# Performance work log

Measured on AMD Instinct MI355X. Metric: run time of the kernel, lower is better.

## Reference

```python
import jax, jax.numpy as jnp
import numpy as np

N = 6000
E = 192000
H = 128
NUM_HEADS = 4

def _segsum(x, idx, n):
    return jax.ops.segment_sum(x, idx, num_segments=n)

def _gcn_encode(x, edges, W0, b0, Ws, bs):
    n = x.shape[0]
    sl = jnp.arange(n, dtype=edges.dtype)
    row = jnp.concatenate([edges[0], sl])  # source
    col = jnp.concatenate([edges[1], sl])  # target (aggregation)
    deg = _segsum(jnp.ones_like(col, dtype=x.dtype), col, n)
    dinv = jax.lax.rsqrt(deg)  # deg >= 1 thanks to self loops
    norm = (dinv[row] * dinv[col])[:, None]
    def layer(h, W, b):
        hw = h @ W
        agg = _segsum(hw[row] * norm, col, n)
        return jax.nn.relu(agg + b)
    h = layer(x, W0, b0)
    for i in range(Ws.shape[0]):
        h = layer(h, Ws[i], bs[i])
    return h

def setup_inputs() -> dict:
    key = jax.random.key(0)
    ks = jax.random.split(key, 24)
    def lin(k, fan_in, shape):
        return jax.random.normal(k, shape, dtype=jnp.float32) / np.sqrt(fan_in)
    return {
        'x_resting': jax.random.normal(ks[0], (N, 3), dtype=jnp.float32),
        'x_rigid': jax.random.normal(ks[1], (N, 3), dtype=jnp.float32),
        'edge_resting': jax.random.randint(ks[2], (2, E), 0, N, dtype=jnp.int32),
        'edge_rigid': jax.random.randint(ks[3], (2, E), 0, N, dtype=jnp.int32),
        'Wr0': lin(ks[4], 3, (3, H)), 'br0': jnp.zeros((H,), jnp.float32),
        'Wr': lin(ks[5], H, (2, H, H)), 'br': jnp.zeros((2, H), jnp.float32),
        'Wg0': lin(ks[6], 3, (3, H)), 'bg0': jnp.zeros((H,), jnp.float32),
        'Wg': lin(ks[7], H, (2, H, H)), 'bg': jnp.zeros((2, H), jnp.float32),
        'Wa': lin(ks[8], H, (NUM_HEADS, H, H)), 'ba': jnp.zeros((NUM_HEADS, H), jnp.float32),
        'Wd0': lin(ks[9], H * (NUM_HEADS + 1), (H * (NUM_HEADS + 1), H)), 'bd0': jnp.zeros((H,), jnp.float32),
        'Wd': lin(ks[10], H, (2, H, H)), 'bd': jnp.zeros((2, H), jnp.float32),
        'Wout': lin(ks[11], H, (H, 3)), 'bout': jnp.zeros((3,), jnp.float32),
    }

def reference(x_resting, x_rigid, edge_resting, edge_rigid,
              Wr0, br0, Wr, br, Wg0, bg0, Wg, bg,
              Wa, ba, Wd0, bd0, Wd, bd, Wout, bout):
    xr = _gcn_encode(x_resting, edge_resting, Wr0, br0, Wr, br)  # (N,H)
    xg = _gcn_encode(x_rigid, edge_rigid, Wg0, bg0, Wg, bg)      # (N,H)

    def head(W, b):
        q = xr @ W + b            # (N,H)
        k = xg @ W + b            # (N,H)
        attn = jax.nn.softmax(q @ k.T, axis=-1)  # (N,N) dense per head
        return attn @ xg          # (N,H)
    heads = jax.vmap(head)(Wa, ba)                       # (heads,N,H)
    pooled = heads.transpose(1, 0, 2).reshape(xr.shape[0], -1)  # (N, heads*H)

    h = jnp.concatenate([xr, pooled], axis=-1)  # (N, H*(heads+1))
    h = jax.nn.relu(h @ Wd0 + bd0)
    for i in range(Wd.shape[0]):
        h = jax.nn.relu(h @ Wd[i] + bd[i])
    return h @ Wout + bout  # (N, 3) deformed positions
```

## Files before the change

### kernel.cpp

```cpp
#include <hip/hip_runtime.h>
#include <math.h>

#define N_NODES 6000
#define N_EDGES 192000
#define H 128
#define NHEADS 4
#define HCAT 640
#define NPAD 6016
#define NTILES 188
#define QBLK 24

typedef unsigned short ushort_t;
typedef __attribute__((ext_vector_type(8))) short short8;
typedef __attribute__((ext_vector_type(16))) float f32x16;

__device__ __forceinline__ void bf16split(float x, ushort_t& hi, ushort_t& lo) {
    unsigned ub = __float_as_uint(x);
    unsigned hb = ub & 0xffff0000u;
    float l = x - __uint_as_float(hb);
    hi = (ushort_t)(hb >> 16);
    lo = (ushort_t)(__float_as_uint(l) >> 16);
}

__device__ __forceinline__ void gll16(const ushort_t* g, ushort_t* l) {
    __builtin_amdgcn_global_load_lds((const __attribute__((address_space(1))) void*)g,
                                     (__attribute__((address_space(3))) void*)l, 16, 0, 0);
}

__global__ void zero_ints(int* p, int n) {
    int i = blockIdx.x * 256 + threadIdx.x;
    if (i < n) p[i] = 0;
}

__global__ void hist2(const int* __restrict__ eA, const int* __restrict__ eB,
                      int* __restrict__ cnt) {
    int e = blockIdx.x * 256 + threadIdx.x;
    int z = blockIdx.y;
    const int* edges = z ? eB : eA;
    if (e < N_EDGES) atomicAdd(&cnt[z * N_NODES + edges[N_EDGES + e]], 1);
}

__global__ __launch_bounds__(1024)
void scan2(const int* __restrict__ cnt_all, int* __restrict__ rs_all) {
    __shared__ int ps[1024];
    int z = blockIdx.x;
    const int* cnt = cnt_all + z * N_NODES;
    int* row_start = rs_all + z * (N_NODES + 1);
    int t = threadIdx.x;
    int base = t * 6;
    int local[6];
    int s = 0;
#pragma unroll
    for (int j = 0; j < 6; ++j) {
        int idx = base + j;
        int v = (idx < N_NODES) ? cnt[idx] : 0;
        local[j] = s;
        s += v;
    }
    ps[t] = s;
    __syncthreads();
    for (int off = 1; off < 1024; off <<= 1) {
        int v = (t >= off) ? ps[t - off] : 0;
        __syncthreads();
        ps[t] += v;
        __syncthreads();
    }
    int ex = (t > 0) ? ps[t - 1] : 0;
#pragma unroll
    for (int j = 0; j < 6; ++j) {
        int idx = base + j;
        if (idx < N_NODES) row_start[idx] = ex + local[j];
    }
    if (t == 1023) row_start[N_NODES] = ps[1023];
}

__global__ void dinv_kernel(const int* __restrict__ cnt, float* __restrict__ dinv, int n) {
    int i = blockIdx.x * 256 + threadIdx.x;
    if (i < n) dinv[i] = rsqrtf((float)(cnt[i] + 1));
}

__global__ void place2(const int* __restrict__ eA, const int* __restrict__ eB,
                       const int* __restrict__ rs_all, int* __restrict__ cur_all,
                       int* __restrict__ eslot_all) {
    int e = blockIdx.x * 256 + threadIdx.x;
    int z = blockIdx.y;
    const int* edges = z ? eB : eA;
    if (e < N_EDGES) {
        int tg = edges[N_EDGES + e];
        int p = atomicAdd(&cur_all[z * N_NODES + tg], 1);
        eslot_all[(size_t)z * N_EDGES + rs_all[z * (N_NODES + 1) + tg] + p] = e;
    }
}

__global__ __launch_bounds__(256)
void gather_x3(const float* __restrict__ xA, const float* __restrict__ xB,
               const int* __restrict__ eA, const int* __restrict__ eB,
               const int* __restrict__ eslot_all, const int* __restrict__ rs_all,
               const float* __restrict__ dinv_all,
               float* __restrict__ outA, float* __restrict__ outB) {
    int z = blockIdx.y;
    int n = blockIdx.x * 256 + threadIdx.x;
    if (n >= N_NODES) return;
    const int* edges = z ? eB : eA;
    const int* eslot = eslot_all + (size_t)z * N_EDGES;
    const int* row_start = rs_all + z * (N_NODES + 1);
    const float* x = z ? xB : xA;
    const float* dv = dinv_all + z * N_NODES;
    float* out = z ? outB : outA;
    float di = dv[n];
    float a0 = x[n * 3 + 0] * di * di;
    float a1 = x[n * 3 + 1] * di * di;
    float a2 = x[n * 3 + 2] * di * di;
    int s0 = row_start[n], s1 = row_start[n + 1];
    for (int i = s0; i < s1; ++i) {
        int e = eslot[i];
        int s = edges[e];
        float nr = dv[s] * di;
        a0 += x[s * 3 + 0] * nr;
        a1 += x[s * 3 + 1] * nr;
        a2 += x[s * 3 + 2] * nr;
    }
    out[n * 3 + 0] = a0; out[n * 3 + 1] = a1; out[n * 3 + 2] = a2;
}

__global__ __launch_bounds__(256)
void gcn_gemm2(const float* __restrict__ hinA, const float* __restrict__ hinB,
               const float* __restrict__ WA, const float* __restrict__ WB,
               float* __restrict__ hwA, float* __restrict__ hwB, int in_dim,
               const float* __restrict__ bA, const float* __restrict__ bB, int do_relu) {
    __shared__ float xs[16 * H];
    int z = blockIdx.y;
    const float* hin = z ? hinB : hinA;
    const float* W = z ? WB : WA;
    float* hw = z ? hwB : hwA;
    const float* b = z ? bB : bA;
    int n0 = blockIdx.x * 16;
    int t = threadIdx.x;
    int f = t & (H - 1);
    int g = t >> 7;
    for (int i = t; i < 16 * H; i += 256) {
        int r = i >> 7, c = i & (H - 1);
        xs[i] = (c < in_dim) ? hin[(size_t)(n0 + r) * in_dim + c] : 0.f;
    }
    __syncthreads();
    float acc[8];
#pragma unroll
    for (int j = 0; j < 8; ++j) acc[j] = 0.f;
    for (int d = 0; d < in_dim; ++d) {
        float w = W[d * H + f];
#pragma unroll
        for (int j = 0; j < 8; ++j) acc[j] += xs[(g * 8 + j) * H + d] * w;
    }
    if (do_relu) {
        float bias = b[f];
#pragma unroll
        for (int j = 0; j < 8; ++j)
            hw[(size_t)(n0 + g * 8 + j) * H + f] = fmaxf(acc[j] + bias, 0.f);
    } else {
#pragma unroll
        for (int j = 0; j < 8; ++j) hw[(size_t)(n0 + g * 8 + j) * H + f] = acc[j];
    }
}

__global__ __launch_bounds__(H)
void gather2(const int* __restrict__ eA, const int* __restrict__ eB,
             const int* __restrict__ eslot_all, const int* __restrict__ rs_all,
             const float* __restrict__ hwA, const float* __restrict__ hwB,
             const float* __restrict__ dinv_all,
             const float* __restrict__ bA, const float* __restrict__ bB,
             float* __restrict__ outA, float* __restrict__ outB, int osA, int osB) {
    __shared__ int ssrc[128];
    __shared__ float snrm[128];
    int z = blockIdx.y;
    const int* edges = z ? eB : eA;
    const int* eslot = eslot_all + (size_t)z * N_EDGES;
    const int* row_start = rs_all + z * (N_NODES + 1);
    const float* hw = z ? hwB : hwA;
    const float* dinv = dinv_all + z * N_NODES;
    const float* b = z ? bB : bA;
    float* out = z ? outB : outA;
    int ostride = z ? osB : osA;

    int tg = blockIdx.x, f = threadIdx.x;
    int s0 = row_start[tg], s1 = row_start[tg + 1];
    float di = dinv[tg];
    float acc = hw[(size_t)tg * H + f] * di * di;
    for (int base = s0; base < s1; base += 128) {
        int cnt = min(128, s1 - base);
        __syncthreads();
        if (f < cnt) {
            int e = eslot[base + f];
            int s = edges[e];
            ssrc[f] = s;
            snrm[f] = dinv[s] * di;
        }
        __syncthreads();
        for (int i = 0; i < cnt; ++i)
            acc += hw[(size_t)ssrc[i] * H + f] * snrm[i];
    }
    float v = acc + b[f];
    out[(size_t)tg * ostride + f] = v > 0.f ? v : 0.f;
}

__global__ __launch_bounds__(256)
void qk_kernel2(const float* __restrict__ qs, int qstride, const float* __restrict__ xg,
                const float* __restrict__ Wa, const float* __restrict__ ba,
                ushort_t* __restrict__ Qh, ushort_t* __restrict__ Ql,
                ushort_t* __restrict__ Khs, ushort_t* __restrict__ Kls) {
    __shared__ float xs[2][16][H];
    int n0 = blockIdx.x * 16, head = blockIdx.y;
    int t = threadIdx.x;
    int f = t & (H - 1);
    int g = t >> 7;
    for (int i = t; i < 2 * 16 * H; i += 256) {
        int which = i >> 11;
        int rem = i & 2047;
        int row = rem >> 7, col = rem & 127;
        xs[which][row][col] = which ? xg[(size_t)(n0 + row) * H + col]
                                    : qs[(size_t)(n0 + row) * qstride + col];
    }
    __syncthreads();
    const float* W = Wa + (size_t)head * H * H;
    float bias = ba[head * H + f];
    float acc[16];
#pragma unroll
    for (int j = 0; j < 16; ++j) acc[j] = bias;
    for (int d = 0; d < H; ++d) {
        float w = W[d * H + f];
#pragma unroll
        for (int j = 0; j < 16; ++j) acc[j] += xs[g][j][d] * w;
    }
#pragma unroll
    for (int j = 0; j < 16; ++j) {
        int n = n0 + j;
        ushort_t hi, lo;
        bf16split(acc[j], hi, lo);
        if (g == 0) {
            size_t idx = ((size_t)(head * N_NODES + n) << 7) + f;
            Qh[idx] = hi; Ql[idx] = lo;
        } else {
            int pos = (((f >> 3) ^ (n & 15)) << 3) + (f & 7);
            size_t idx = ((size_t)(head * NPAD + n) << 7) + pos;
            Khs[idx] = hi; Kls[idx] = lo;
        }
    }
}

__global__ void zero_pad_k(ushort_t* __restrict__ Khs, ushort_t* __restrict__ Kls) {
    int i = blockIdx.x * 256 + threadIdx.x;
    if (i < NHEADS * 16 * H) {
        int head = i / (16 * H);
        int rest = i - head * 16 * H;
        int n = N_NODES + (rest >> 7);
        int f = rest & 127;
        size_t idx = ((size_t)(head * NPAD + n) << 7) + f;
        Khs[idx] = 0; Kls[idx] = 0;
    }
}

__global__ __launch_bounds__(128)
void cvt_vt(const float* __restrict__ xg, ushort_t* __restrict__ Vth, ushort_t* __restrict__ Vtl) {
    __shared__ float vs[32][129];
    int t0 = blockIdx.x;
    int t = threadIdx.x;
    for (int c = t; c < 32 * 32; c += 128) {
        int row = c >> 5, col4 = (c & 31) << 2;
        int n = t0 * 32 + row;
        float4 v = (n < N_NODES) ? *(const float4*)&xg[(size_t)n * H + col4]
                                 : float4{0.f, 0.f, 0.f, 0.f};
        vs[row][col4 + 0] = v.x; vs[row][col4 + 1] = v.y;
        vs[row][col4 + 2] = v.z; vs[row][col4 + 3] = v.w;
    }
    __syncthreads();
    int d = t;
    size_t base = ((size_t)t0 * H + d) * 32;
#pragma unroll
    for (int oc = 0; oc < 4; ++oc) {
        int cc = oc ^ (d & 3);
        unsigned uh[4], ul[4];
#pragma unroll
        for (int j = 0; j < 4; ++j) {
            ushort_t h0, l0, h1, l1;
            bf16split(vs[cc * 8 + 2 * j][d], h0, l0);
            bf16split(vs[cc * 8 + 2 * j + 1][d], h1, l1);
            uh[j] = (unsigned)h0 | ((unsigned)h1 << 16);
            ul[j] = (unsigned)l0 | ((unsigned)l1 << 16);
        }
        *(uint4*)&Vth[base + oc * 8] = make_uint4(uh[0], uh[1], uh[2], uh[3]);
        *(uint4*)&Vtl[base + oc * 8] = make_uint4(ul[0], ul[1], ul[2], ul[3]);
    }
}

__global__ __launch_bounds__(512, 2)
void attn_mfma5(const ushort_t* __restrict__ Qh, const ushort_t* __restrict__ Ql,
                const ushort_t* __restrict__ Khs, const ushort_t* __restrict__ Kls,
                const ushort_t* __restrict__ Vth, const ushort_t* __restrict__ Vtl,
                float* __restrict__ Opart, float* __restrict__ mlpart, int tps) {
    __shared__ ushort_t lds[2][4][4096];
    const int head = blockIdx.y;
    const int sp = blockIdx.z;
    const int t = threadIdx.x;
    const int lane = t & 63;
    const int w = t >> 6;
    const int r = lane & 31;
    const int h = lane >> 5;
    const int q0w = blockIdx.x * 256 + w * 32;

    int t_begin = sp * tps;
    int t_end = t_begin + tps; if (t_end > NTILES) t_end = NTILES;

    const size_t kbase = (size_t)head * NPAD * H;
    const int lo8 = t * 8;

    int qr = q0w + r; if (qr > N_NODES - 1) qr = N_NODES - 1;
    const size_t qbase = ((size_t)(head * N_NODES + qr)) << 7;
    short8 qfh[8], qfl[8];
#pragma unroll
    for (int s = 0; s < 8; ++s) {
        qfh[s] = *(const short8*)&Qh[qbase + 16 * s + 8 * h];
        qfl[s] = *(const short8*)&Ql[qbase + 16 * s + 8 * h];
    }

    f32x16 O[4];
#pragma unroll
    for (int sub = 0; sub < 4; ++sub)
#pragma unroll
        for (int i = 0; i < 16; ++i) O[sub][i] = 0.f;
    float mrun = -1e30f, lrun = 0.f;

    {
        size_t off = (size_t)t_begin * 4096 + lo8;
        gll16(Khs + kbase + off, &lds[0][0][lo8]);
        gll16(Kls + kbase + off, &lds[0][1][lo8]);
        gll16(Vth + off, &lds[0][2][lo8]);
        gll16(Vtl + off, &lds[0][3][lo8]);
    }

    for (int it = t_begin; it < t_end; ++it) {
        const int b = (it - t_begin) & 1;
        __syncthreads();
        {
            int nt = it + 1; if (nt >= t_end) nt = t_begin;
            size_t off = (size_t)nt * 4096 + lo8;
            gll16(Khs + kbase + off, &lds[b ^ 1][0][lo8]);
            gll16(Kls + kbase + off, &lds[b ^ 1][1][lo8]);
            gll16(Vth + off, &lds[b ^ 1][2][lo8]);
            gll16(Vtl + off, &lds[b ^ 1][3][lo8]);
        }
        const ushort_t* lKh = &lds[b][0][0];
        const ushort_t* lKl = &lds[b][1][0];
        const ushort_t* lVh = &lds[b][2][0];
        const ushort_t* lVl = &lds[b][3][0];

        f32x16 acc;
#pragma unroll
        for (int i = 0; i < 16; ++i) acc[i] = 0.f;
        const int krow = r * H;
#pragma unroll
        for (int s = 0; s < 8; ++s) {
            int cc = ((2 * s + h) ^ (r & 15)) << 3;
            short8 ah = *(const short8*)&lKh[krow + cc];
            short8 al = *(const short8*)&lKl[krow + cc];
            acc = __builtin_amdgcn_mfma_f32_32x32x16_bf16(ah, qfh[s], acc, 0, 0, 0);
            acc = __builtin_amdgcn_mfma_f32_32x32x16_bf16(ah, qfl[s], acc, 0, 0, 0);
            acc = __builtin_amdgcn_mfma_f32_32x32x16_bf16(al, qfh[s], acc, 0, 0, 0);
        }

        float sv[16];
#pragma unroll
        for (int i = 0; i < 16; ++i) sv[i] = acc[i];
        int klim = N_NODES - (it << 5);
        if (klim < 32) {
#pragma unroll
            for (int i = 0; i < 16; ++i) {
                int row = (i & 3) + 8 * (i >> 2) + 4 * h;
                if (row >= klim) sv[i] = -1e30f;
            }
        }
        float tmax = sv[0];
#pragma unroll
        for (int i = 1; i < 16; ++i) tmax = fmaxf(tmax, sv[i]);
        tmax = fmaxf(tmax, __shfl_xor(tmax, 32));
        float mnew = fmaxf(mrun, tmax);
        float p[16];
        float psum = 0.f;
#pragma unroll
        for (int i = 0; i < 16; ++i) { p[i] = __expf(sv[i] - mnew); psum += p[i]; }

        if (__ballot(mnew > mrun)) {
            float alpha = __expf(mrun - mnew);
            lrun *= alpha;
#pragma unroll
            for (int i = 0; i < 16; ++i) {
                int rowq = (i & 3) + 8 * (i >> 2) + 4 * h;
                float a = __shfl(alpha, rowq);
#pragma unroll
                for (int sub = 0; sub < 4; ++sub) O[sub][i] *= a;
            }
        }
        lrun += psum;
        mrun = mnew;

        float pr[16];
#pragma unroll
        for (int i = 0; i < 16; ++i) pr[i] = __shfl_xor(p[i], 32);
        short8 aPh[2], aPl[2];
#pragma unroll
        for (int s2 = 0; s2 < 2; ++s2) {
#pragma unroll
            for (int j = 0; j < 8; ++j) {
                int c = j & 3;
                float v;
                if (j < 4) v = (h == 0) ? p[c + 8 * s2] : pr[c + 8 * s2 + 4];
                else       v = (h == 1) ? p[c + 8 * s2 + 4] : pr[c + 8 * s2];
                unsigned ub = __float_as_uint(v);
                unsigned hb = ub & 0xffff0000u;
                float lo = v - __uint_as_float(hb);
                aPh[s2][j] = (short)(hb >> 16);
                aPl[s2][j] = (short)(__float_as_uint(lo) >> 16);
            }
        }

#pragma unroll
        for (int sub = 0; sub < 4; ++sub) {
            const int vrow = (32 * sub + r) * 32;
#pragma unroll
            for (int s2 = 0; s2 < 2; ++s2) {
                int cc = (((2 * s2 + h) ^ (r & 3)) << 3);
                short8 bh = *(const short8*)&lVh[vrow + cc];
                short8 bl = *(const short8*)&lVl[vrow + cc];
                O[sub] = __builtin_amdgcn_mfma_f32_32x32x16_bf16(aPh[s2], bh, O[sub], 0, 0, 0);
                O[sub] = __builtin_amdgcn_mfma_f32_32x32x16_bf16(aPh[s2], bl, O[sub], 0, 0, 0);
                O[sub] = __builtin_amdgcn_mfma_f32_32x32x16_bf16(aPl[s2], bh, O[sub], 0, 0, 0);
            }
        }
    }

    lrun += __shfl_xor(lrun, 32);

    float* Ob = Opart + (size_t)(sp * NHEADS + head) * NPAD * H;
#pragma unroll
    for (int i = 0; i < 16; ++i) {
        int rowq = (i & 3) + 8 * (i >> 2) + 4 * h;
        int qg = q0w + rowq;
        if (qg < N_NODES) {
            float* dst = &Ob[(size_t)qg * H + r];
#pragma unroll
            for (int sub = 0; sub < 4; ++sub) dst[32 * sub] = O[sub][i];
        }
    }
    if (h == 0 && q0w + r < N_NODES) {
        float2* ml = (float2*)mlpart;
        ml[(size_t)(sp * NHEADS + head) * NPAD + q0w + r] = make_float2(mrun, lrun);
    }
}

__global__ __launch_bounds__(256)
void attn_combine(const float* __restrict__ Opart, const float* __restrict__ mlpart,
                  float* __restrict__ hcat, int ns) {
    int idx = blockIdx.x * 256 + threadIdx.x;
    if (idx >= NHEADS * N_NODES * (H / 4)) return;
    int head = idx / (N_NODES * (H / 4));
    int rest = idx - head * N_NODES * (H / 4);
    int q = rest >> 5;
    int d4 = (rest & 31) << 2;
    const float2* ml = (const float2*)mlpart;
    float m = -1e30f;
    for (int s = 0; s < ns; ++s)
        m = fmaxf(m, ml[(size_t)(s * NHEADS + head) * NPAD + q].x);
    float lsum = 0.f;
    float4 o = {0.f, 0.f, 0.f, 0.f};
    for (int s = 0; s < ns; ++s) {
        float2 v = ml[(size_t)(s * NHEADS + head) * NPAD + q];
        float wgt = __expf(v.x - m);
        lsum += v.y * wgt;
        float4 ov = *(const float4*)&Opart[((size_t)(s * NHEADS + head) * NPAD + q) * H + d4];
        o.x += ov.x * wgt; o.y += ov.y * wgt; o.z += ov.z * wgt; o.w += ov.w * wgt;
    }
    float inv = 1.f / lsum;
    float4 res = {o.x * inv, o.y * inv, o.z * inv, o.w * inv};
    *(float4*)&hcat[(size_t)q * HCAT + H + head * H + d4] = res;
}

__global__ __launch_bounds__(256)
void decoder(const float* __restrict__ hcat,
             const float* __restrict__ Wd0, const float* __restrict__ bd0,
             const float* __restrict__ Wd, const float* __restrict__ bd,
             const float* __restrict__ Wout, const float* __restrict__ bout,
             float* __restrict__ out) {
    __shared__ float s0[8 * HCAT];
    __shared__ float s1[8 * H];
    __shared__ float s2[8 * H];
    int n0 = blockIdx.x * 8;
    int t = threadIdx.x;
    int f = t & (H - 1);
    int g = t >> 7;
    for (int i = t; i < 8 * HCAT; i += 256)
        s0[i] = hcat[(size_t)n0 * HCAT + i];
    __syncthreads();

    float acc[4];
#pragma unroll
    for (int j = 0; j < 4; ++j) acc[j] = bd0[f];
    for (int d = 0; d < HCAT; ++d) {
        float w = Wd0[d * H + f];
#pragma unroll
        for (int j = 0; j < 4; ++j) acc[j] += s0[(g * 4 + j) * HCAT + d] * w;
    }
#pragma unroll
    for (int j = 0; j < 4; ++j) s1[(g * 4 + j) * H + f] = fmaxf(acc[j], 0.f);
    __syncthreads();

#pragma unroll
    for (int j = 0; j < 4; ++j) acc[j] = bd[f];
    for (int d = 0; d < H; ++d) {
        float w = Wd[d * H + f];
#pragma unroll
        for (int j = 0; j < 4; ++j) acc[j] += s1[(g * 4 + j) * H + d] * w;
    }
#pragma unroll
    for (int j = 0; j < 4; ++j) s2[(g * 4 + j) * H + f] = fmaxf(acc[j], 0.f);
    __syncthreads();

#pragma unroll
    for (int j = 0; j < 4; ++j) acc[j] = bd[H + f];
    for (int d = 0; d < H; ++d) {
        float w = Wd[H * H + d * H + f];
#pragma unroll
        for (int j = 0; j < 4; ++j) acc[j] += s2[(g * 4 + j) * H + d] * w;
    }
    __syncthreads();
#pragma unroll
    for (int j = 0; j < 4; ++j) s1[(g * 4 + j) * H + f] = fmaxf(acc[j], 0.f);
    __syncthreads();

    if (t < 24) {
        int n = t / 3, c = t % 3;
        float o = bout[c];
        for (int d = 0; d < H; ++d) o += s1[n * H + d] * Wout[d * 3 + c];
        out[(size_t)(n0 + n) * 3 + c] = o;
    }
}

extern "C" void kernel_launch(void* const* d_in, const int* in_sizes, int n_in,
                              void* d_out, int out_size, void* d_ws, size_t ws_size,
                              hipStream_t stream) {
    const float* x_rest = (const float*)d_in[0];
    const float* x_rig  = (const float*)d_in[1];
    const int*   e_rest = (const int*)d_in[2];
    const int*   e_rig  = (const int*)d_in[3];
    const float* Wr0 = (const float*)d_in[4];
    const float* br0 = (const float*)d_in[5];
    const float* Wr  = (const float*)d_in[6];
    const float* br  = (const float*)d_in[7];
    const float* Wg0 = (const float*)d_in[8];
    const float* bg0 = (const float*)d_in[9];
    const float* Wg  = (const float*)d_in[10];
    const float* bg  = (const float*)d_in[11];
    const float* Wa  = (const float*)d_in[12];
    const float* ba  = (const float*)d_in[13];
    const float* Wd0 = (const float*)d_in[14];
    const float* bd0 = (const float*)d_in[15];
    const float* Wd  = (const float*)d_in[16];
    const float* bd  = (const float*)d_in[17];
    const float* Wout = (const float*)d_in[18];
    const float* bout = (const float*)d_in[19];
    float* out = (float*)d_out;

    const size_t NH = (size_t)N_NODES * H;
    float* ws = (float*)d_ws;
    float* dinv = ws;
    float* hw   = dinv + 2 * N_NODES;
    float* hb   = hw + 2 * NH;
    float* hcat = hb + 2 * NH;
    float* ha   = hcat;
    float* xg   = hb + NH;
    float* xagg = hb;
    ushort_t* Qh  = (ushort_t*)(hcat + (size_t)N_NODES * HCAT);
    ushort_t* Ql  = Qh + (size_t)NHEADS * N_NODES * H;
    ushort_t* Khs = Ql + (size_t)NHEADS * N_NODES * H;
    ushort_t* Kls = Khs + (size_t)NHEADS * NPAD * H;
    ushort_t* Vth = Kls + (size_t)NHEADS * NPAD * H;
    ushort_t* Vtl = Vth + (size_t)NTILES * H * 32;
    int* ib   = (int*)(Vtl + (size_t)NTILES * H * 32);
    int* cnt  = ib;
    int* cur  = cnt + 2 * N_NODES;
    int* rs   = cur + 2 * N_NODES;
    int* eslot = rs + 2 * (N_NODES + 1);
    int* iend  = eslot + 2 * N_EDGES;
    float* Opart = (float*)(((uintptr_t)iend + 15) & ~(uintptr_t)15);

    size_t base_bytes = (size_t)((char*)Opart - (char*)d_ws);
    size_t per_split  = (size_t)NHEADS * NPAD * (H + 2) * sizeof(float);
    int NS = 2;
    if (ws_size >= base_bytes + 5 * per_split + (1u << 20)) NS = 5;
    else if (ws_size >= base_bytes + 4 * per_split + (1u << 20)) NS = 4;
    float* mlpart = Opart + (size_t)NS * NHEADS * NPAD * H;
    int tps = (NTILES + NS - 1) / NS;

    const int gN = (N_NODES + 255) / 256;
    const int gE = (N_EDGES + 255) / 256;

    zero_ints<<<(4 * N_NODES + 255) / 256, 256, 0, stream>>>(cnt, 4 * N_NODES);
    hist2<<<dim3(gE, 2), 256, 0, stream>>>(e_rest, e_rig, cnt);
    scan2<<<2, 1024, 0, stream>>>(cnt, rs);
    dinv_kernel<<<(2 * N_NODES + 255) / 256, 256, 0, stream>>>(cnt, dinv, 2 * N_NODES);
    place2<<<dim3(gE, 2), 256, 0, stream>>>(e_rest, e_rig, rs, cur, eslot);

    float* hw_r = hw, * hw_g = hw + NH;
    float* ha_r = ha, * ha_g = ha + NH;
    float* hb_r = hb, * hb_g = hb + NH;
    float* xagg_r = xagg, * xagg_g = xagg + 3 * N_NODES;

    gather_x3<<<dim3(gN, 2), 256, 0, stream>>>(x_rest, x_rig, e_rest, e_rig, eslot, rs,
                                               dinv, xagg_r, xagg_g);
    gcn_gemm2<<<dim3(N_NODES / 16, 2), 256, 0, stream>>>(xagg_r, xagg_g, Wr0, Wg0,
                                                         ha_r, ha_g, 3, br0, bg0, 1);
    gcn_gemm2<<<dim3(N_NODES / 16, 2), 256, 0, stream>>>(ha_r, ha_g, Wr, Wg, hw_r, hw_g, H,
                                                         nullptr, nullptr, 0);
    gather2<<<dim3(N_NODES, 2), H, 0, stream>>>(e_rest, e_rig, eslot, rs, hw_r, hw_g, dinv,
                                                br, bg, hb_r, hb_g, H, H);
    gcn_gemm2<<<dim3(N_NODES / 16, 2), 256, 0, stream>>>(hb_r, hb_g, Wr + H * H, Wg + H * H,
                                                         hw_r, hw_g, H, nullptr, nullptr, 0);
    gather2<<<dim3(N_NODES, 2), H, 0, stream>>>(e_rest, e_rig, eslot, rs, hw_r, hw_g, dinv,
                                                br + H, bg + H, hcat, xg, HCAT, H);

    qk_kernel2<<<dim3(N_NODES / 16, NHEADS), 256, 0, stream>>>(hcat, HCAT, xg, Wa, ba,
                                                               Qh, Ql, Khs, Kls);
    zero_pad_k<<<(NHEADS * 16 * H + 255) / 256, 256, 0, stream>>>(Khs, Kls);
    cvt_vt<<<NTILES, 128, 0, stream>>>(xg, Vth, Vtl);
    attn_mfma5<<<dim3(QBLK, NHEADS, NS), 512, 0, stream>>>(Qh, Ql, Khs, Kls, Vth, Vtl,
                                                           Opart, mlpart, tps);
    attn_combine<<<(NHEADS * N_NODES * (H / 4) + 255) / 256, 256, 0, stream>>>(Opart, mlpart,
                                                                               hcat, NS);

    decoder<<<N_NODES / 8, 256, 0, stream>>>(hcat, Wd0, bd0, Wd, bd, Wout, bout, out);
}
```

Measured before the change: 614.2 us.

## Load V fragments directly to registers and halve attention block size

The attention kernel now keeps only K in double-buffered LDS. V is stored pre-swizzled in MFMA B-operand fragment order and loaded straight into registers, one tile ahead, instead of going through LDS. Blocks shrink from 512 to 256 threads, giving 47 query blocks per head, and the conversion kernel writes the new V layout. The dinv computation is also folded into the scan kernel to drop one launch. This cuts LDS traffic and footprint per block, but adds 16 short8 registers per thread for V and issues global loads per wave for the same V tile.

Result: no change. 617.2 us (+0.5%).

```diff
diff --git a/kernel.cpp b/kernel.cpp
--- a/kernel.cpp
+++ b/kernel.cpp
@@ -8,7 +8,6 @@
 #define HCAT 640
 #define NPAD 6016
 #define NTILES 188
-#define QBLK 24
 
 typedef unsigned short ushort_t;
 typedef __attribute__((ext_vector_type(8))) short short8;
@@ -41,11 +40,13 @@
 }
 
 __global__ __launch_bounds__(1024)
-void scan2(const int* __restrict__ cnt_all, int* __restrict__ rs_all) {
+void scan2(const int* __restrict__ cnt_all, int* __restrict__ rs_all,
+           float* __restrict__ dinv_all) {
     __shared__ int ps[1024];
     int z = blockIdx.x;
     const int* cnt = cnt_all + z * N_NODES;
     int* row_start = rs_all + z * (N_NODES + 1);
+    float* dinv = dinv_all + z * N_NODES;
     int t = threadIdx.x;
     int base = t * 6;
     int local[6];
@@ -56,6 +57,7 @@
         int v = (idx < N_NODES) ? cnt[idx] : 0;
         local[j] = s;
         s += v;
+        if (idx < N_NODES) dinv[idx] = rsqrtf((float)(v + 1));
     }
     ps[t] = s;
     __syncthreads();
@@ -72,11 +74,6 @@
         if (idx < N_NODES) row_start[idx] = ex + local[j];
     }
     if (t == 1023) row_start[N_NODES] = ps[1023];
-}
-
-__global__ void dinv_kernel(const int* __restrict__ cnt, float* __restrict__ dinv, int n) {
-    int i = blockIdx.x * 256 + threadIdx.x;
-    if (i < n) dinv[i] = rsqrtf((float)(cnt[i] + 1));
 }
 
 __global__ void place2(const int* __restrict__ eA, const int* __restrict__ eB,
@@ -258,12 +255,12 @@
     }
 }
 
-__global__ __launch_bounds__(128)
-void cvt_vt(const float* __restrict__ xg, ushort_t* __restrict__ Vth, ushort_t* __restrict__ Vtl) {
-    __shared__ float vs[32][129];
+__global__ __launch_bounds__(256)
+void cvt_vt2(const float* __restrict__ xg, ushort_t* __restrict__ Vth, ushort_t* __restrict__ Vtl) {
+    __shared__ float vs[32][132];
     int t0 = blockIdx.x;
     int t = threadIdx.x;
-    for (int c = t; c < 32 * 32; c += 128) {
+    for (int c = t; c < 32 * 32; c += 256) {
         int row = c >> 5, col4 = (c & 31) << 2;
         int n = t0 * 32 + row;
         float4 v = (n < N_NODES) ? *(const float4*)&xg[(size_t)n * H + col4]
@@ -272,31 +269,30 @@
         vs[row][col4 + 2] = v.z; vs[row][col4 + 3] = v.w;
     }
     __syncthreads();
-    int d = t;
-    size_t base = ((size_t)t0 * H + d) * 32;
-#pragma unroll
-    for (int oc = 0; oc < 4; ++oc) {
-        int cc = oc ^ (d & 3);
-        unsigned uh[4], ul[4];
-#pragma unroll
-        for (int j = 0; j < 4; ++j) {
-            ushort_t h0, l0, h1, l1;
-            bf16split(vs[cc * 8 + 2 * j][d], h0, l0);
-            bf16split(vs[cc * 8 + 2 * j + 1][d], h1, l1);
-            uh[j] = (unsigned)h0 | ((unsigned)h1 << 16);
-            ul[j] = (unsigned)l0 | ((unsigned)l1 << 16);
-        }
-        *(uint4*)&Vth[base + oc * 8] = make_uint4(uh[0], uh[1], uh[2], uh[3]);
-        *(uint4*)&Vtl[base + oc * 8] = make_uint4(ul[0], ul[1], ul[2], ul[3]);
-    }
-}
-
-__global__ __launch_bounds__(512, 2)
-void attn_mfma5(const ushort_t* __restrict__ Qh, const ushort_t* __restrict__ Ql,
+    for (int sl = t; sl < 512; sl += 256) {
+        int sub = sl >> 7;
+        int s2 = (sl >> 6) & 1;
+        int lane = sl & 63;
+        int r = lane & 31, hh = lane >> 5;
+        int d = 32 * sub + r;
+        ushort_t oh[8], ol[8];
+#pragma unroll
+        for (int j = 0; j < 8; ++j) {
+            int k = (2 * s2 + hh) * 8 + j;
+            bf16split(vs[k][d], oh[j], ol[j]);
+        }
+        size_t base = (size_t)t0 * 4096 + (size_t)sl * 8;
+        *(short8*)&Vth[base] = *(short8*)oh;
+        *(short8*)&Vtl[base] = *(short8*)ol;
+    }
+}
+
+__global__ __launch_bounds__(256, 2)
+void attn_mfma6(const ushort_t* __restrict__ Qh, const ushort_t* __restrict__ Ql,
                 const ushort_t* __restrict__ Khs, const ushort_t* __restrict__ Kls,
                 const ushort_t* __restrict__ Vth, const ushort_t* __restrict__ Vtl,
                 float* __restrict__ Opart, float* __restrict__ mlpart, int tps) {
-    __shared__ ushort_t lds[2][4][4096];
+    __shared__ ushort_t Kbuf[2][2][4096];
     const int head = blockIdx.y;
     const int sp = blockIdx.z;
     const int t = threadIdx.x;
@@ -304,13 +300,13 @@
     const int w = t >> 6;
     const int r = lane & 31;
     const int h = lane >> 5;
-    const int q0w = blockIdx.x * 256 + w * 32;
+    const int q0w = blockIdx.x * 128 + w * 32;
 
     int t_begin = sp * tps;
     int t_end = t_begin + tps; if (t_end > NTILES) t_end = NTILES;
 
     const size_t kbase = (size_t)head * NPAD * H;
-    const int lo8 = t * 8;
+    const int o1 = t * 8, o2 = t * 8 + 2048;
 
     int qr = q0w + r; if (qr > N_NODES - 1) qr = N_NODES - 1;
     const size_t qbase = ((size_t)(head * N_NODES + qr)) << 7;
@@ -329,11 +325,20 @@
     float mrun = -1e30f, lrun = 0.f;
 
     {
-        size_t off = (size_t)t_begin * 4096 + lo8;
-        gll16(Khs + kbase + off, &lds[0][0][lo8]);
-        gll16(Kls + kbase + off, &lds[0][1][lo8]);
-        gll16(Vth + off, &lds[0][2][lo8]);
-        gll16(Vtl + off, &lds[0][3][lo8]);
+        const ushort_t* sKh = Khs + kbase + (size_t)t_begin * 4096;
+        const ushort_t* sKl = Kls + kbase + (size_t)t_begin * 4096;
+        gll16(sKh + o1, &Kbuf[0][0][o1]); gll16(sKh + o2, &Kbuf[0][0][o2]);
+        gll16(sKl + o1, &Kbuf[0][1][o1]); gll16(sKl + o2, &Kbuf[0][1][o2]);
+    }
+    short8 vh[8], vl[8];
+    {
+        const ushort_t* vbh = Vth + (size_t)t_begin * 4096 + lane * 8;
+        const ushort_t* vbl = Vtl + (size_t)t_begin * 4096 + lane * 8;
+#pragma unroll
+        for (int i = 0; i < 8; ++i) {
+            vh[i] = *(const short8*)(vbh + i * 512);
+            vl[i] = *(const short8*)(vbl + i * 512);
+        }
     }
 
     for (int it = t_begin; it < t_end; ++it) {
@@ -341,16 +346,13 @@
         __syncthreads();
         {
             int nt = it + 1; if (nt >= t_end) nt = t_begin;
-            size_t off = (size_t)nt * 4096 + lo8;
-            gll16(Khs + kbase + off, &lds[b ^ 1][0][lo8]);
-            gll16(Kls + kbase + off, &lds[b ^ 1][1][lo8]);
-            gll16(Vth + off, &lds[b ^ 1][2][lo8]);
-            gll16(Vtl + off, &lds[b ^ 1][3][lo8]);
-        }
-        const ushort_t* lKh = &lds[b][0][0];
-        const ushort_t* lKl = &lds[b][1][0];
-        const ushort_t* lVh = &lds[b][2][0];
-        const ushort_t* lVl = &lds[b][3][0];
+            const ushort_t* sKh = Khs + kbase + (size_t)nt * 4096;
+            const ushort_t* sKl = Kls + kbase + (size_t)nt * 4096;
+            gll16(sKh + o1, &Kbuf[b ^ 1][0][o1]); gll16(sKh + o2, &Kbuf[b ^ 1][0][o2]);
+            gll16(sKl + o1, &Kbuf[b ^ 1][1][o1]); gll16(sKl + o2, &Kbuf[b ^ 1][1][o2]);
+        }
+        const ushort_t* lKh = &Kbuf[b][0][0];
+        const ushort_t* lKl = &Kbuf[b][1][0];
 
         f32x16 acc;
 #pragma unroll
@@ -423,15 +425,24 @@
 
 #pragma unroll
         for (int sub = 0; sub < 4; ++sub) {
-            const int vrow = (32 * sub + r) * 32;
 #pragma unroll
             for (int s2 = 0; s2 < 2; ++s2) {
-                int cc = (((2 * s2 + h) ^ (r & 3)) << 3);
-                short8 bh = *(const short8*)&lVh[vrow + cc];
-                short8 bl = *(const short8*)&lVl[vrow + cc];
+                short8 bh = vh[sub * 2 + s2];
+                short8 bl = vl[sub * 2 + s2];
                 O[sub] = __builtin_amdgcn_mfma_f32_32x32x16_bf16(aPh[s2], bh, O[sub], 0, 0, 0);
                 O[sub] = __builtin_amdgcn_mfma_f32_32x32x16_bf16(aPh[s2], bl, O[sub], 0, 0, 0);
                 O[sub] = __builtin_amdgcn_mfma_f32_32x32x16_bf16(aPl[s2], bh, O[sub], 0, 0, 0);
+            }
+        }
+
+        {
+            int nt = it + 1; if (nt >= t_end) nt = t_begin;
+            const ushort_t* vbh = Vth + (size_t)nt * 4096 + lane * 8;
+            const ushort_t* vbl = Vtl + (size_t)nt * 4096 + lane * 8;
+#pragma unroll
+            for (int i = 0; i < 8; ++i) {
+                vh[i] = *(const short8*)(vbh + i * 512);
+                vl[i] = *(const short8*)(vbl + i * 512);
             }
         }
     }
@@ -603,8 +614,7 @@
 
     zero_ints<<<(4 * N_NODES + 255) / 256, 256, 0, stream>>>(cnt, 4 * N_NODES);
     hist2<<<dim3(gE, 2), 256, 0, stream>>>(e_rest, e_rig, cnt);
-    scan2<<<2, 1024, 0, stream>>>(cnt, rs);
-    dinv_kernel<<<(2 * N_NODES + 255) / 256, 256, 0, stream>>>(cnt, dinv, 2 * N_NODES);
+    scan2<<<2, 1024, 0, stream>>>(cnt, rs, dinv);
     place2<<<dim3(gE, 2), 256, 0, stream>>>(e_rest, e_rig, rs, cur, eslot);
 
     float* hw_r = hw, * hw_g = hw + NH;
@@ -628,9 +638,9 @@
     qk_kernel2<<<dim3(N_NODES / 16, NHEADS), 256, 0, stream>>>(hcat, HCAT, xg, Wa, ba,
                                                                Qh, Ql, Khs, Kls);
     zero_pad_k<<<(NHEADS * 16 * H + 255) / 256, 256, 0, stream>>>(Khs, Kls);
-    cvt_vt<<<NTILES, 128, 0, stream>>>(xg, Vth, Vtl);
-    attn_mfma5<<<dim3(QBLK, NHEADS, NS), 512, 0, stream>>>(Qh, Ql, Khs, Kls, Vth, Vtl,
-                                                           Opart, mlpart, tps);
+    cvt_vt2<<<NTILES, 256, 0, stream>>>(xg, Vth, Vtl);
+    attn_mfma6<<<dim3(47, NHEADS, NS), 256, 0, stream>>>(Qh, Ql, Khs, Kls, Vth, Vtl,
+                                                         Opart, mlpart, tps);
     attn_combine<<<(NHEADS * N_NODES * (H / 4) + 255) / 256, 256, 0, stream>>>(Opart, mlpart,
                                                                                hcat, NS);
 
```

## Software-pipeline attention PV step one tile behind QK and halve block size

Applied to the files above, without the earlier changes.

The attention kernel now issues the P·V MFMAs for the previous key tile after the current tile's QK MFMAs, deferring the softmax rescale of O to that point, so the exp/softmax latency overlaps with matrix work. Blocks shrink from 512 to 256 threads (128 queries each, 47 blocks per head-split), with each thread loading two 16-byte chunks per buffer. V tiles are loaded one iteration later to match the deferred use. Separately, the dinv computation is folded into the scan kernel to drop one launch. The trade is extra live registers for the P fragments and alpha, plus the extra grid blocks re-reading K/V tiles.

New measurement: 610.9 us. Within noise of the previous version (-0.5%).

```diff
diff --git a/kernel.cpp b/kernel.cpp
--- a/kernel.cpp
+++ b/kernel.cpp
@@ -8,7 +8,6 @@
 #define HCAT 640
 #define NPAD 6016
 #define NTILES 188
-#define QBLK 24
 
 typedef unsigned short ushort_t;
 typedef __attribute__((ext_vector_type(8))) short short8;
@@ -41,11 +40,13 @@
 }
 
 __global__ __launch_bounds__(1024)
-void scan2(const int* __restrict__ cnt_all, int* __restrict__ rs_all) {
+void scan2(const int* __restrict__ cnt_all, int* __restrict__ rs_all,
+           float* __restrict__ dinv_all) {
     __shared__ int ps[1024];
     int z = blockIdx.x;
     const int* cnt = cnt_all + z * N_NODES;
     int* row_start = rs_all + z * (N_NODES + 1);
+    float* dinv = dinv_all + z * N_NODES;
     int t = threadIdx.x;
     int base = t * 6;
     int local[6];
@@ -56,6 +57,7 @@
         int v = (idx < N_NODES) ? cnt[idx] : 0;
         local[j] = s;
         s += v;
+        if (idx < N_NODES) dinv[idx] = rsqrtf((float)(v + 1));
     }
     ps[t] = s;
     __syncthreads();
@@ -72,11 +74,6 @@
         if (idx < N_NODES) row_start[idx] = ex + local[j];
     }
     if (t == 1023) row_start[N_NODES] = ps[1023];
-}
-
-__global__ void dinv_kernel(const int* __restrict__ cnt, float* __restrict__ dinv, int n) {
-    int i = blockIdx.x * 256 + threadIdx.x;
-    if (i < n) dinv[i] = rsqrtf((float)(cnt[i] + 1));
 }
 
 __global__ void place2(const int* __restrict__ eA, const int* __restrict__ eB,
@@ -291,8 +288,8 @@
     }
 }
 
-__global__ __launch_bounds__(512, 2)
-void attn_mfma5(const ushort_t* __restrict__ Qh, const ushort_t* __restrict__ Ql,
+__global__ __launch_bounds__(256, 2)
+void attn_mfma7(const ushort_t* __restrict__ Qh, const ushort_t* __restrict__ Ql,
                 const ushort_t* __restrict__ Khs, const ushort_t* __restrict__ Kls,
                 const ushort_t* __restrict__ Vth, const ushort_t* __restrict__ Vtl,
                 float* __restrict__ Opart, float* __restrict__ mlpart, int tps) {
@@ -304,13 +301,13 @@
     const int w = t >> 6;
     const int r = lane & 31;
     const int h = lane >> 5;
-    const int q0w = blockIdx.x * 256 + w * 32;
+    const int q0w = blockIdx.x * 128 + w * 32;
 
     int t_begin = sp * tps;
     int t_end = t_begin + tps; if (t_end > NTILES) t_end = NTILES;
 
     const size_t kbase = (size_t)head * NPAD * H;
-    const int lo8 = t * 8;
+    const int o1 = t * 8, o2 = t * 8 + 2048;
 
     int qr = q0w + r; if (qr > N_NODES - 1) qr = N_NODES - 1;
     const size_t qbase = ((size_t)(head * N_NODES + qr)) << 7;
@@ -327,13 +324,15 @@
 #pragma unroll
         for (int i = 0; i < 16; ++i) O[sub][i] = 0.f;
     float mrun = -1e30f, lrun = 0.f;
+    short8 aPh[2], aPl[2];
+    float alpha_prev = 1.f;
+    int resc_prev = 0;
 
     {
-        size_t off = (size_t)t_begin * 4096 + lo8;
-        gll16(Khs + kbase + off, &lds[0][0][lo8]);
-        gll16(Kls + kbase + off, &lds[0][1][lo8]);
-        gll16(Vth + off, &lds[0][2][lo8]);
-        gll16(Vtl + off, &lds[0][3][lo8]);
+        const ushort_t* sKh = Khs + kbase + (size_t)t_begin * 4096;
+        const ushort_t* sKl = Kls + kbase + (size_t)t_begin * 4096;
+        gll16(sKh + o1, &lds[0][0][o1]); gll16(sKh + o2, &lds[0][0][o2]);
+        gll16(sKl + o1, &lds[0][1][o1]); gll16(sKl + o2, &lds[0][1][o2]);
     }
 
     for (int it = t_begin; it < t_end; ++it) {
@@ -341,11 +340,14 @@
         __syncthreads();
         {
             int nt = it + 1; if (nt >= t_end) nt = t_begin;
-            size_t off = (size_t)nt * 4096 + lo8;
-            gll16(Khs + kbase + off, &lds[b ^ 1][0][lo8]);
-            gll16(Kls + kbase + off, &lds[b ^ 1][1][lo8]);
-            gll16(Vth + off, &lds[b ^ 1][2][lo8]);
-            gll16(Vtl + off, &lds[b ^ 1][3][lo8]);
+            const ushort_t* sKh = Khs + kbase + (size_t)nt * 4096;
+            const ushort_t* sKl = Kls + kbase + (size_t)nt * 4096;
+            const ushort_t* sVh = Vth + (size_t)it * 4096;
+            const ushort_t* sVl = Vtl + (size_t)it * 4096;
+            gll16(sKh + o1, &lds[b ^ 1][0][o1]); gll16(sKh + o2, &lds[b ^ 1][0][o2]);
+            gll16(sKl + o1, &lds[b ^ 1][1][o1]); gll16(sKl + o2, &lds[b ^ 1][1][o2]);
+            gll16(sVh + o1, &lds[b ^ 1][2][o1]); gll16(sVh + o2, &lds[b ^ 1][2][o2]);
+            gll16(sVl + o1, &lds[b ^ 1][3][o1]); gll16(sVl + o2, &lds[b ^ 1][3][o2]);
         }
         const ushort_t* lKh = &lds[b][0][0];
         const ushort_t* lKl = &lds[b][1][0];
@@ -366,6 +368,31 @@
             acc = __builtin_amdgcn_mfma_f32_32x32x16_bf16(al, qfh[s], acc, 0, 0, 0);
         }
 
+        if (it != t_begin) {
+            if (resc_prev) {
+#pragma unroll
+                for (int i = 0; i < 16; ++i) {
+                    int rowq = (i & 3) + 8 * (i >> 2) + 4 * h;
+                    float a = __shfl(alpha_prev, rowq);
+#pragma unroll
+                    for (int sub = 0; sub < 4; ++sub) O[sub][i] *= a;
+                }
+            }
+#pragma unroll
+            for (int sub = 0; sub < 4; ++sub) {
+                const int vrow = (32 * sub + r) * 32;
+#pragma unroll
+                for (int s2 = 0; s2 < 2; ++s2) {
+                    int cc = (((2 * s2 + h) ^ (r & 3)) << 3);
+                    short8 bh = *(const short8*)&lVh[vrow + cc];
+                    short8 bl = *(const short8*)&lVl[vrow + cc];
+                    O[sub] = __builtin_amdgcn_mfma_f32_32x32x16_bf16(aPh[s2], bh, O[sub], 0, 0, 0);
+                    O[sub] = __builtin_amdgcn_mfma_f32_32x32x16_bf16(aPh[s2], bl, O[sub], 0, 0, 0);
+                    O[sub] = __builtin_amdgcn_mfma_f32_32x32x16_bf16(aPl[s2], bh, O[sub], 0, 0, 0);
+                }
+            }
+        }
+
         float sv[16];
 #pragma unroll
         for (int i = 0; i < 16; ++i) sv[i] = acc[i];
@@ -390,13 +417,10 @@
         if (__ballot(mnew > mrun)) {
             float alpha = __expf(mrun - mnew);
             lrun *= alpha;
-#pragma unroll
-            for (int i = 0; i < 16; ++i) {
-                int rowq = (i & 3) + 8 * (i >> 2) + 4 * h;
-                float a = __shfl(alpha, rowq);
-#pragma unroll
-                for (int sub = 0; sub < 4; ++sub) O[sub][i] *= a;
-            }
+            alpha_prev = alpha;
+            resc_prev = 1;
+        } else {
+            resc_prev = 0;
         }
         lrun += psum;
         mrun = mnew;
@@ -404,7 +428,6 @@
         float pr[16];
 #pragma unroll
         for (int i = 0; i < 16; ++i) pr[i] = __shfl_xor(p[i], 32);
-        short8 aPh[2], aPl[2];
 #pragma unroll
         for (int s2 = 0; s2 < 2; ++s2) {
 #pragma unroll
@@ -420,7 +443,22 @@
                 aPl[s2][j] = (short)(__float_as_uint(lo) >> 16);
             }
         }
-
+    }
+
+    __syncthreads();
+    {
+        const int bl = (t_end - t_begin) & 1;
+        const ushort_t* lVh = &lds[bl][2][0];
+        const ushort_t* lVl = &lds[bl][3][0];
+        if (resc_prev) {
+#pragma unroll
+            for (int i = 0; i < 16; ++i) {
+                int rowq = (i & 3) + 8 * (i >> 2) + 4 * h;
+                float a = __shfl(alpha_prev, rowq);
+#pragma unroll
+                for (int sub = 0; sub < 4; ++sub) O[sub][i] *= a;
+            }
+        }
 #pragma unroll
         for (int sub = 0; sub < 4; ++sub) {
             const int vrow = (32 * sub + r) * 32;
@@ -603,8 +641,7 @@
 
     zero_ints<<<(4 * N_NODES + 255) / 256, 256, 0, stream>>>(cnt, 4 * N_NODES);
     hist2<<<dim3(gE, 2), 256, 0, stream>>>(e_rest, e_rig, cnt);
-    scan2<<<2, 1024, 0, stream>>>(cnt, rs);
-    dinv_kernel<<<(2 * N_NODES + 255) / 256, 256, 0, stream>>>(cnt, dinv, 2 * N_NODES);
+    scan2<<<2, 1024, 0, stream>>>(cnt, rs, dinv);
     place2<<<dim3(gE, 2), 256, 0, stream>>>(e_rest, e_rig, rs, cur, eslot);
 
     float* hw_r = hw, * hw_g = hw + NH;
@@ -629,8 +666,8 @@
                                                                Qh, Ql, Khs, Kls);
     zero_pad_k<<<(NHEADS * 16 * H + 255) / 256, 256, 0, stream>>>(Khs, Kls);
     cvt_vt<<<NTILES, 128, 0, stream>>>(xg, Vth, Vtl);
-    attn_mfma5<<<dim3(QBLK, NHEADS, NS), 512, 0, stream>>>(Qh, Ql, Khs, Kls, Vth, Vtl,
-                                                           Opart, mlpart, tps);
+    attn_mfma7<<<dim3(47, NHEADS, NS), 256, 0, stream>>>(Qh, Ql, Khs, Kls, Vth, Vtl,
+                                                         Opart, mlpart, tps);
     attn_combine<<<(NHEADS * N_NODES * (H / 4) + 255) / 256, 256, 0, stream>>>(Opart, mlpart,
                                                                                hcat, NS);
 
```
